# Kernel optimization log

Measured on AMD Instinct MI355X. Metric: run time of the kernel, lower is better.

Reference implementation:

```python
import jax, jax.numpy as jnp
import numpy as np

# ---- module geometry ----
BULK = 64          # bulk (J2) integration points, 3 comps each
COH = 32           # cohesive integration points, 2 comps each
LS = BULK * 3 + COH * 2  # = 256, material layer width

# ---- J2 plasticity material constants (plane-stress, linear isotropic hardening) ----
E_MOD = 200.0
NU = 0.3
SY0 = 2.0
HARD = 10.0
G_MOD = E_MOD / (2.0 * (1.0 + NU))
_c = E_MOD / (1.0 - NU * NU)
C_EL = np.array([[_c, _c * NU, 0.0], [_c * NU, _c, 0.0], [0.0, 0.0, _c * (1.0 - NU) / 2.0]], dtype=np.float32)
C_INV = np.linalg.inv(C_EL).astype(np.float32)

# ---- Turon cohesive-zone constants (bilinear damage law) ----
K_PEN = 50.0       # penalty stiffness
DELTA0 = 0.1       # damage-onset effective jump
DELTAF = 1.0       # full-failure effective jump


def j2_update(eps, epsp, epbar):
    # eps, epsp: [B,P,3]; epbar: [B,P]. Radial-return with linear hardening.
    sig_tr = jnp.einsum('bpi,ji->bpj', eps - epsp, jnp.asarray(C_EL))
    s1, s2, s12 = sig_tr[..., 0], sig_tr[..., 1], sig_tr[..., 2]
    seq = jnp.sqrt(jnp.maximum(s1 * s1 - s1 * s2 + s2 * s2 + 3.0 * s12 * s12, 1e-12))
    f = seq - (SY0 + HARD * epbar)
    plastic = f > 0.0
    dep = jnp.where(plastic, f / (3.0 * G_MOD + HARD), 0.0)
    r = (SY0 + HARD * (epbar + dep)) / seq
    sig = jnp.where(plastic[..., None], r[..., None] * sig_tr, sig_tr)
    epsp_new = jnp.where(plastic[..., None], eps - jnp.einsum('bpj,ij->bpi', sig, jnp.asarray(C_INV)), epsp)
    return sig, epsp_new, epbar + dep


def coh_update(jump, hist):
    # jump: [B,P,2] (normal, shear); hist: [B,P] max effective jump (damage history).
    dn, ds = jump[..., 0], jump[..., 1]
    lam = jnp.sqrt(jnp.maximum(jnp.maximum(dn, 0.0) ** 2 + ds * ds, 1e-12))
    hist_new = jnp.maximum(hist, lam)
    dmg = jnp.clip(DELTAF * (hist_new - DELTA0) / (jnp.maximum(hist_new, 1e-12) * (DELTAF - DELTA0)), 0.0, 1.0)
    tn = K_PEN * dn * jnp.where(dn > 0.0, 1.0 - dmg, 1.0)  # compression is undamaged
    ts = (1.0 - dmg) * K_PEN * ds
    return jnp.stack([tn, ts], axis=-1), hist_new


def setup_inputs() -> dict:
    key = jax.random.key(0)
    k1, k2, k3 = jax.random.split(key, 3)
    x = jax.random.normal(k1, (256, 1024, 16), dtype=jnp.float32)
    W1 = jax.random.normal(k2, (LS, 16), dtype=jnp.float32) * 0.1
    W2 = jax.random.normal(k3, (16, LS), dtype=jnp.float32) * 0.1
    return {"x": x, "W1": W1, "W2": W2}


def reference(x, W1, W2):
    B, T, F = x.shape
    # fc1 applied to every (batch, time) slice (original loops; here one GEMM)
    h = jnp.einsum('btf,lf->btl', x, W1)  # [B,T,LS]
    h_t = jnp.transpose(h, (1, 0, 2))     # [T,B,LS] for the time scan

    epsp0 = jnp.zeros((B, BULK, 3), dtype=x.dtype)
    epbar0 = jnp.zeros((B, BULK), dtype=x.dtype)
    hist0 = jnp.zeros((B, COH), dtype=x.dtype)

    def step(carry, ht):
        epsp, epbar, hist = carry
        eps = ht[:, : BULK * 3].reshape(B, BULK, 3)
        jmp = ht[:, BULK * 3:].reshape(B, COH, 2)
        sig, epsp, epbar = j2_update(eps, epsp, epbar)   # update + commit per step
        trac, hist = coh_update(jmp, hist)
        y = jnp.concatenate([sig.reshape(B, -1), trac.reshape(B, -1)], axis=-1)
        return (epsp, epbar, hist), y

    _, ys = jax.lax.scan(step, (epsp0, epbar0, hist0), h_t)  # [T,B,LS]
    ys = jnp.transpose(ys, (1, 0, 2))  # [B,T,LS]
    # softLayer fc2: linear with softplus-constrained (non-negative) weights
    out = jnp.einsum('btl,ol->bto', ys, jax.nn.softplus(W2))
    return out
```

## Files before the change

kernel.cpp:

```cpp
#include <hip/hip_runtime.h>
#include <cmath>
#include <cstdint>

#define BATCH  256
#define TT     1024
#define FIN    16
#define TC     32
#define NCHUNK (TT / TC)
#define SROW   324
#define YSS    328
#define HB     16

typedef __attribute__((ext_vector_type(8))) short short8;
typedef __attribute__((ext_vector_type(4))) float floatx4;

__device__ __forceinline__ unsigned short f2bf_rne(float f) {
    union { float f; unsigned int i; } v; v.f = f;
    unsigned int b = v.i;
    return (unsigned short)((b + 0x7FFFu + ((b >> 16) & 1u)) >> 16);
}
__device__ __forceinline__ float u2f(unsigned int u) {
    union { unsigned int i; float f; } v; v.i = u; return v.f;
}

#define BARRIER() asm volatile("s_waitcnt lgkmcnt(0)\n\ts_barrier" ::: "memory")
#define SBAR()    __builtin_amdgcn_sched_barrier(0)

#define MC00   219.78021978021977f
#define MC01   65.93406593406593f
#define MC22   76.92307692307692f
#define MSY0   2.0f
#define AK     0.958466453674121406f
#define BK     0.041533546325878594f


__global__ __launch_bounds__(512, 2)
void fused_mat_kernel(const float* __restrict__ x,
                      const float* __restrict__ w1,
                      const float* __restrict__ w2,
                      float* __restrict__ out)
{
    __shared__ __attribute__((aligned(16))) float          s_h[2][TC][SROW];
    __shared__ __attribute__((aligned(16))) unsigned short s_y[2][TC][YSS];

    const int tid  = threadIdx.x;
    const int b    = blockIdx.x;
    const int lane = tid & 63;
    const int wv   = tid >> 6;
    const int m    = lane & 15;
    const int q    = lane >> 4;

    const size_t xrow = (size_t)b * TT;

    const bool isG   = (wv == 2) | (wv == 3) | (wv == 6) | (wv == 7);
    const int  hw    = (wv == 2) ? 0 : (wv == 3) ? 1 : (wv == 6) ? 2 : 3;
    const int  nbase = hw * 5;

    short8 wfrag[5];
    short8 vf[10];
    uint4  rxc[2][2], rxp[2][2];

    auto emit = [&](const short8* axv, const short8* adxv, float* dst) {
        #pragma unroll
        for (int mt = 0; mt < 2; ++mt) {
            float* drow = dst + (mt * 16 + m) * SROW + q * 4 + nbase * 16;
            #pragma unroll
            for (int j = 0; j < 5; ++j) {
                const int n = nbase + j;
                floatx4 acc = {0.f, 0.f, 0.f, 0.f};
                acc = __builtin_amdgcn_mfma_f32_16x16x32_bf16(
                        wfrag[j], (n < 16) ? adxv[mt] : axv[mt], acc, 0, 0, 0);
                *(floatx4*)(drow + j * 16) = acc;
            }
        }
    };

    if (isG) {
        #pragma unroll
        for (int j = 0; j < 5; ++j) {
            const int n = nbase + j;
            #pragma unroll
            for (int jj = 0; jj < 8; ++jj) {
                float v = 0.f;
                if (q < 2) {
                    const int f = q * 8 + jj;
                    if (n < 16) {
                        const int lp = n * 16 + m, c = lp >> 2, cm = lp & 3;
                        if (cm < 3) {
                            const float wa  = w1[(3 * c + 0) * FIN + f];
                            const float wb  = w1[(3 * c + 1) * FIN + f];
                            const float wcc = w1[(3 * c + 2) * FIN + f];
                            v = (cm == 0) ? fmaf(MC01, wb, MC00 * wa)
                              : (cm == 1) ? fmaf(MC00, wb, MC01 * wa)
                                          : MC22 * wcc;
                        }
                    } else {
                        v = w1[(192 + (n - 16) * 16 + m) * FIN + f];
                    }
                }
                wfrag[j][jj] = (short)f2bf_rne(v);
            }
        }
        short8 ax0[2], adx0[2];
        #pragma unroll
        for (int mt = 0; mt < 2; ++mt) {
            #pragma unroll
            for (int j = 0; j < 8; ++j) {
                float xc = 0.f, xp = 0.f;
                if (q < 2) {
                    const int rowB = mt * 16 + m;
                    xc = x[(xrow + rowB) * FIN + q * 8 + j];
                    if (rowB > 0) xp = x[(xrow + rowB - 1) * FIN + q * 8 + j];
                }
                ax0[mt][j]  = (short)f2bf_rne(xc);
                adx0[mt][j] = (short)f2bf_rne(xc - xp);
            }
        }
        if (q < 2) {
            #pragma unroll
            for (int mt = 0; mt < 2; ++mt) {
                const int rowB = TC + mt * 16 + m;
                const float* xc = x + (xrow + rowB) * FIN + q * 8;
                const float* xp = x + (xrow + rowB - 1) * FIN + q * 8;
                rxc[mt][0] = *(const uint4*)xc;  rxc[mt][1] = *(const uint4*)(xc + 4);
                rxp[mt][0] = *(const uint4*)xp;  rxp[mt][1] = *(const uint4*)(xp + 4);
            }
        }
        emit(ax0, adx0, &s_h[0][0][0]);
    } else if (wv == 4 || wv == 5) {
        #pragma unroll
        for (int ks = 0; ks < 10; ++ks) {
            #pragma unroll
            for (int j = 0; j < 8; ++j) {
                const int p = ks * 32 + q * 8 + j;
                unsigned short v = 0;
                if (p < 256) {
                    const int comp = p & 3;
                    if (comp < 3) {
                        const int l = 3 * (p >> 2) + comp;
                        float xv = w2[m * 256 + l];
                        float sp = fmaxf(xv, 0.0f) + log1pf(expf(-fabsf(xv)));
                        v = f2bf_rne(sp);
                    }
                } else {
                    const int l = p - 64;
                    float xv = w2[m * 256 + l];
                    float sp = fmaxf(xv, 0.0f) + log1pf(expf(-fabsf(xv)));
                    v = f2bf_rne(sp);
                }
                vf[ks][j] = (short)v;
            }
        }
    }

    float tt0 = 0.f, tt1 = 0.f, tt2 = 0.f, rr = 1.0f, syv = MSY0, pre = AK * MSY0;
    float hist = 0.f;

    __syncthreads();

    for (int i = 0; i <= NCHUNK; ++i) {
        if (wv == 0) {
            if (i < NCHUNK) {
                const float* hb = &s_h[i & 1][0][0] + 4 * lane;
                unsigned short* yb = &s_y[i & 1][0][0] + 4 * lane;
                floatx4 dvvA[HB], dvvB[HB];
                uint2   yreg[TC];
                #pragma unroll
                for (int t = 0; t < HB; ++t) dvvA[t] = *(const floatx4*)(hb + t * SROW);
                SBAR();
                #pragma unroll
                for (int t = 0; t < HB; ++t) dvvB[t] = *(const floatx4*)(hb + (HB + t) * SROW);
                SBAR();
                #pragma unroll
                for (int t = 0; t < TC; ++t) {
                    const floatx4 dv = (t < HB) ? dvvA[t] : dvvB[t - HB];
                    tt0 = fmaf(rr, tt0, dv.x);
                    tt1 = fmaf(rr, tt1, dv.y);
                    tt2 = fmaf(rr, tt2, dv.z);
                    const float s01 = tt0 - tt1;
                    const float u   = tt2 * tt2;
                    const float w3  = fmaf(u, 3.0f, 1e-12f);
                    const float bb  = fmaf(tt1, tt1, w3);
                    const float qq  = fmaf(tt0, s01, bb);
                    const float rs  = __builtin_amdgcn_rsqf(qq);
                    const float seq = qq * rs;
                    rr  = fminf(fmaf(pre, rs, BK), 1.0f);
                    syv = fmaxf(syv, fmaf(BK, seq, pre));
                    pre = AK * syv;
                    const float sg0 = rr * tt0, sg1 = rr * tt1, sg2 = rr * tt2;
                    unsigned int r0, r1;
                    asm("v_cvt_pk_bf16_f32 %0, %1, %2" : "=v"(r0) : "v"(sg0), "v"(sg1));
                    asm("v_cvt_pk_bf16_f32 %0, %1, %2" : "=v"(r1) : "v"(sg2), "v"(sg2));
                    yreg[t].x = r0; yreg[t].y = r1;
                }
                SBAR();
                #pragma unroll
                for (int t = 0; t < TC; ++t)
                    *(uint2*)(yb + t * YSS) = yreg[t];
            }
        } else if (wv == 1) {
            if (i < NCHUNK && lane < 32) {
                const float* hc = &s_h[i & 1][0][0] + 256 + 2 * lane;
                unsigned short* yc = &s_y[i & 1][0][0] + 256 + 2 * lane;
                float2 jvv[TC];
                unsigned int yr[TC];
                #pragma unroll
                for (int t = 0; t < TC; ++t) jvv[t] = *(const float2*)(hc + t * SROW);
                SBAR();
                #pragma unroll
                for (int t = 0; t < TC; ++t) {
                    const float dn = jvv[t].x, ds = jvv[t].y;
                    const float dnp = fmaxf(dn, 0.0f);
                    const float lam = __builtin_amdgcn_sqrtf(fmaxf(fmaf(dnp, dnp, ds * ds), 1e-12f));
                    hist = fmaxf(hist, lam);
                    float dmg = (hist - 0.1f) * __builtin_amdgcn_rcpf(hist * 0.9f);
                    dmg = fminf(fmaxf(dmg, 0.0f), 1.0f);
                    const float om = 1.0f - dmg;
                    const float tn = 50.0f * dn * (dn > 0.0f ? om : 1.0f);
                    const float ts = om * 50.0f * ds;
                    unsigned int r;
                    asm("v_cvt_pk_bf16_f32 %0, %1, %2" : "=v"(r) : "v"(tn), "v"(ts));
                    yr[t] = r;
                }
                SBAR();
                #pragma unroll
                for (int t = 0; t < TC; ++t)
                    *(unsigned int*)(yc + t * YSS) = yr[t];
            }
        } else if (isG) {
            if (i + 1 < NCHUNK) {
                short8 ax[2], adx[2];
                #pragma unroll
                for (int mt = 0; mt < 2; ++mt) {
                    const unsigned int wc[8] = {rxc[mt][0].x, rxc[mt][0].y, rxc[mt][0].z, rxc[mt][0].w,
                                                rxc[mt][1].x, rxc[mt][1].y, rxc[mt][1].z, rxc[mt][1].w};
                    const unsigned int wp[8] = {rxp[mt][0].x, rxp[mt][0].y, rxp[mt][0].z, rxp[mt][0].w,
                                                rxp[mt][1].x, rxp[mt][1].y, rxp[mt][1].z, rxp[mt][1].w};
                    union { unsigned int u[4]; short8 s; } Ua, Ud;
                    #pragma unroll
                    for (int p = 0; p < 4; ++p) {
                        const float c0 = u2f(wc[2 * p]),          c1 = u2f(wc[2 * p + 1]);
                        const float d0 = c0 - u2f(wp[2 * p]),     d1 = c1 - u2f(wp[2 * p + 1]);
                        unsigned int va, vd;
                        asm("v_cvt_pk_bf16_f32 %0, %1, %2" : "=v"(va) : "v"(c0), "v"(c1));
                        asm("v_cvt_pk_bf16_f32 %0, %1, %2" : "=v"(vd) : "v"(d0), "v"(d1));
                        Ua.u[p] = (q < 2) ? va : 0u;
                        Ud.u[p] = (q < 2) ? vd : 0u;
                    }
                    ax[mt]  = Ua.s;
                    adx[mt] = Ud.s;
                }
                if (i + 2 < NCHUNK && q < 2) {
                    #pragma unroll
                    for (int mt = 0; mt < 2; ++mt) {
                        const int rowB = (i + 2) * TC + mt * 16 + m;
                        const float* xc = x + (xrow + rowB) * FIN + q * 8;
                        const float* xp = x + (xrow + rowB - 1) * FIN + q * 8;
                        rxc[mt][0] = *(const uint4*)xc;  rxc[mt][1] = *(const uint4*)(xc + 4);
                        rxp[mt][0] = *(const uint4*)xp;  rxp[mt][1] = *(const uint4*)(xp + 4);
                    }
                }
                emit(ax, adx, &s_h[(i + 1) & 1][0][0]);
            }
        } else {
            if (i >= 1) {
                const int mt = wv - 4;
                const int tb = (i - 1) * TC;
                const unsigned short* yb = &s_y[(i - 1) & 1][0][0];
                floatx4 a0 = {0.f, 0.f, 0.f, 0.f};
                floatx4 a1 = {0.f, 0.f, 0.f, 0.f};
                #pragma unroll
                for (int ks = 0; ks < 5; ++ks) {
                    const short8* yp = (const short8*)(yb + (mt * 16 + m) * YSS + ks * 32 + q * 8);
                    a0 = __builtin_amdgcn_mfma_f32_16x16x32_bf16(*yp, vf[ks], a0, 0, 0, 0);
                }
                #pragma unroll
                for (int ks = 5; ks < 10; ++ks) {
                    const short8* yp = (const short8*)(yb + (mt * 16 + m) * YSS + ks * 32 + q * 8);
                    a1 = __builtin_amdgcn_mfma_f32_16x16x32_bf16(*yp, vf[ks], a1, 0, 0, 0);
                }
                #pragma unroll
                for (int r = 0; r < 4; ++r)
                    out[(xrow + tb + mt * 16 + q * 4 + r) * FIN + m] = a0[r] + a1[r];
            }
        }
        BARRIER();
    }
}

extern "C" void kernel_launch(void* const* d_in, const int* in_sizes, int n_in,
                              void* d_out, int out_size, void* d_ws, size_t ws_size,
                              hipStream_t stream) {
    const float* x  = (const float*)d_in[0];
    const float* w1 = (const float*)d_in[1];
    const float* w2 = (const float*)d_in[2];
    float* out = (float*)d_out;
    fused_mat_kernel<<<BATCH, 512, 0, stream>>>(x, w1, w2, out);
}
```

Baseline: 140.7 us.

## Replace per-chunk block barriers with LDS flag-based producer/consumer sync

Each wave role gets its own loop, and the block-wide barrier every chunk is replaced by LDS flags that producers set and consumers spin on. The serial J2 wave can start its next chunk as soon as the input tile and the free output buffer are ready, instead of waiting for the slowest role. The risk is fragile memory ordering: only a compiler fence is used on the acquire side and an lgkmcnt wait on the release side. Spinning waves also compete for issue slots.

```diff
diff --git a/kernel.cpp b/kernel.cpp
--- a/kernel.cpp
+++ b/kernel.cpp
@@ -23,8 +23,9 @@
     union { unsigned int i; float f; } v; v.i = u; return v.f;
 }
 
-#define BARRIER() asm volatile("s_waitcnt lgkmcnt(0)\n\ts_barrier" ::: "memory")
-#define SBAR()    __builtin_amdgcn_sched_barrier(0)
+#define SBAR()  __builtin_amdgcn_sched_barrier(0)
+#define ACQ()   asm volatile("" ::: "memory")
+#define REL()   asm volatile("s_waitcnt lgkmcnt(0)" ::: "memory")
 
 #define MC00   219.78021978021977f
 #define MC01   65.93406593406593f
@@ -42,6 +43,9 @@
 {
     __shared__ __attribute__((aligned(16))) float          s_h[2][TC][SROW];
     __shared__ __attribute__((aligned(16))) unsigned short s_y[2][TC][YSS];
+    __shared__ int flg[16];
+
+    volatile int* F = (volatile int*)flg;
 
     const int tid  = threadIdx.x;
     const int b    = blockIdx.x;
@@ -59,6 +63,10 @@
     short8 wfrag[5];
     short8 vf[10];
     uint4  rxc[2][2], rxp[2][2];
+
+    if (tid == 0) {
+        flg[4] = -1; flg[5] = -1; flg[6] = -1; flg[7] = -1; flg[8] = -1; flg[9] = -1;
+    }
 
     auto emit = [&](const short8* axv, const short8* adxv, float* dst) {
         #pragma unroll
@@ -127,6 +135,7 @@
             }
         }
         emit(ax0, adx0, &s_h[0][0][0]);
+        if (lane == 0) flg[hw] = 0;
     } else if (wv == 4 || wv == 5) {
         #pragma unroll
         for (int ks = 0; ks < 10; ++ks) {
@@ -158,48 +167,58 @@
 
     __syncthreads();
 
-    for (int i = 0; i <= NCHUNK; ++i) {
-        if (wv == 0) {
-            if (i < NCHUNK) {
-                const float* hb = &s_h[i & 1][0][0] + 4 * lane;
-                unsigned short* yb = &s_y[i & 1][0][0] + 4 * lane;
-                floatx4 dvvA[HB], dvvB[HB];
-                uint2   yreg[TC];
-                #pragma unroll
-                for (int t = 0; t < HB; ++t) dvvA[t] = *(const floatx4*)(hb + t * SROW);
-                SBAR();
-                #pragma unroll
-                for (int t = 0; t < HB; ++t) dvvB[t] = *(const floatx4*)(hb + (HB + t) * SROW);
-                SBAR();
-                #pragma unroll
-                for (int t = 0; t < TC; ++t) {
-                    const floatx4 dv = (t < HB) ? dvvA[t] : dvvB[t - HB];
-                    tt0 = fmaf(rr, tt0, dv.x);
-                    tt1 = fmaf(rr, tt1, dv.y);
-                    tt2 = fmaf(rr, tt2, dv.z);
-                    const float s01 = tt0 - tt1;
-                    const float u   = tt2 * tt2;
-                    const float w3  = fmaf(u, 3.0f, 1e-12f);
-                    const float bb  = fmaf(tt1, tt1, w3);
-                    const float qq  = fmaf(tt0, s01, bb);
-                    const float rs  = __builtin_amdgcn_rsqf(qq);
-                    const float seq = qq * rs;
-                    rr  = fminf(fmaf(pre, rs, BK), 1.0f);
-                    syv = fmaxf(syv, fmaf(BK, seq, pre));
-                    pre = AK * syv;
-                    const float sg0 = rr * tt0, sg1 = rr * tt1, sg2 = rr * tt2;
-                    unsigned int r0, r1;
-                    asm("v_cvt_pk_bf16_f32 %0, %1, %2" : "=v"(r0) : "v"(sg0), "v"(sg1));
-                    asm("v_cvt_pk_bf16_f32 %0, %1, %2" : "=v"(r1) : "v"(sg2), "v"(sg2));
-                    yreg[t].x = r0; yreg[t].y = r1;
-                }
-                SBAR();
-                #pragma unroll
-                for (int t = 0; t < TC; ++t)
-                    *(uint2*)(yb + t * YSS) = yreg[t];
-            }
-        } else if (wv == 1) {
-            if (i < NCHUNK && lane < 32) {
+    if (wv == 0) {
+        for (int i = 0; i < NCHUNK; ++i) {
+            while (F[0] < i) {} while (F[1] < i) {} while (F[2] < i) {} while (F[3] < i) {}
+            const int yf = i - 2;
+            while (F[8] < yf) {} while (F[9] < yf) {}
+            ACQ();
+            const float* hb = &s_h[i & 1][0][0] + 4 * lane;
+            unsigned short* yb = &s_y[i & 1][0][0] + 4 * lane;
+            floatx4 dvvA[HB], dvvB[HB];
+            uint2   yreg[TC];
+            #pragma unroll
+            for (int t = 0; t < HB; ++t) dvvA[t] = *(const floatx4*)(hb + t * SROW);
+            SBAR();
+            #pragma unroll
+            for (int t = 0; t < HB; ++t) dvvB[t] = *(const floatx4*)(hb + (HB + t) * SROW);
+            SBAR();
+            #pragma unroll
+            for (int t = 0; t < TC; ++t) {
+                const floatx4 dv = (t < HB) ? dvvA[t] : dvvB[t - HB];
+                tt0 = fmaf(rr, tt0, dv.x);
+                tt1 = fmaf(rr, tt1, dv.y);
+                tt2 = fmaf(rr, tt2, dv.z);
+                const float s01 = tt0 - tt1;
+                const float u   = tt2 * tt2;
+                const float w3  = fmaf(u, 3.0f, 1e-12f);
+                const float bb  = fmaf(tt1, tt1, w3);
+                const float qq  = fmaf(tt0, s01, bb);
+                const float rs  = __builtin_amdgcn_rsqf(qq);
+                const float seq = qq * rs;
+                rr  = fminf(fmaf(pre, rs, BK), 1.0f);
+                syv = fmaxf(syv, fmaf(BK, seq, pre));
+                pre = AK * syv;
+                const float sg0 = rr * tt0, sg1 = rr * tt1, sg2 = rr * tt2;
+                unsigned int r0, r1;
+                asm("v_cvt_pk_bf16_f32 %0, %1, %2" : "=v"(r0) : "v"(sg0), "v"(sg1));
+                asm("v_cvt_pk_bf16_f32 %0, %1, %2" : "=v"(r1) : "v"(sg2), "v"(sg2));
+                yreg[t].x = r0; yreg[t].y = r1;
+            }
+            SBAR();
+            #pragma unroll
+            for (int t = 0; t < TC; ++t)
+                *(uint2*)(yb + t * YSS) = yreg[t];
+            REL();
+            if (lane == 0) { F[4] = i; F[6] = i; }
+        }
+    } else if (wv == 1) {
+        for (int i = 0; i < NCHUNK; ++i) {
+            while (F[3] < i) {}
+            const int yf = i - 2;
+            while (F[8] < yf) {} while (F[9] < yf) {}
+            ACQ();
+            if (lane < 32) {
                 const float* hc = &s_h[i & 1][0][0] + 256 + 2 * lane;
                 unsigned short* yc = &s_y[i & 1][0][0] + 256 + 2 * lane;
                 float2 jvv[TC];
@@ -227,64 +246,76 @@
                 for (int t = 0; t < TC; ++t)
                     *(unsigned int*)(yc + t * YSS) = yr[t];
             }
-        } else if (isG) {
-            if (i + 1 < NCHUNK) {
-                short8 ax[2], adx[2];
+            REL();
+            if (lane == 0) { F[5] = i; F[7] = i; }
+        }
+    } else if (isG) {
+        for (int k = 1; k < NCHUNK; ++k) {
+            short8 ax[2], adx[2];
+            #pragma unroll
+            for (int mt = 0; mt < 2; ++mt) {
+                const unsigned int wc[8] = {rxc[mt][0].x, rxc[mt][0].y, rxc[mt][0].z, rxc[mt][0].w,
+                                            rxc[mt][1].x, rxc[mt][1].y, rxc[mt][1].z, rxc[mt][1].w};
+                const unsigned int wp[8] = {rxp[mt][0].x, rxp[mt][0].y, rxp[mt][0].z, rxp[mt][0].w,
+                                            rxp[mt][1].x, rxp[mt][1].y, rxp[mt][1].z, rxp[mt][1].w};
+                union { unsigned int u[4]; short8 s; } Ua, Ud;
+                #pragma unroll
+                for (int p = 0; p < 4; ++p) {
+                    const float c0 = u2f(wc[2 * p]),          c1 = u2f(wc[2 * p + 1]);
+                    const float d0 = c0 - u2f(wp[2 * p]),     d1 = c1 - u2f(wp[2 * p + 1]);
+                    unsigned int va, vd;
+                    asm("v_cvt_pk_bf16_f32 %0, %1, %2" : "=v"(va) : "v"(c0), "v"(c1));
+                    asm("v_cvt_pk_bf16_f32 %0, %1, %2" : "=v"(vd) : "v"(d0), "v"(d1));
+                    Ua.u[p] = (q < 2) ? va : 0u;
+                    Ud.u[p] = (q < 2) ? vd : 0u;
+                }
+                ax[mt]  = Ua.s;
+                adx[mt] = Ud.s;
+            }
+            if (k + 1 < NCHUNK && q < 2) {
                 #pragma unroll
                 for (int mt = 0; mt < 2; ++mt) {
-                    const unsigned int wc[8] = {rxc[mt][0].x, rxc[mt][0].y, rxc[mt][0].z, rxc[mt][0].w,
-                                                rxc[mt][1].x, rxc[mt][1].y, rxc[mt][1].z, rxc[mt][1].w};
-                    const unsigned int wp[8] = {rxp[mt][0].x, rxp[mt][0].y, rxp[mt][0].z, rxp[mt][0].w,
-                                                rxp[mt][1].x, rxp[mt][1].y, rxp[mt][1].z, rxp[mt][1].w};
-                    union { unsigned int u[4]; short8 s; } Ua, Ud;
-                    #pragma unroll
-                    for (int p = 0; p < 4; ++p) {
-                        const float c0 = u2f(wc[2 * p]),          c1 = u2f(wc[2 * p + 1]);
-                        const float d0 = c0 - u2f(wp[2 * p]),     d1 = c1 - u2f(wp[2 * p + 1]);
-                        unsigned int va, vd;
-                        asm("v_cvt_pk_bf16_f32 %0, %1, %2" : "=v"(va) : "v"(c0), "v"(c1));
-                        asm("v_cvt_pk_bf16_f32 %0, %1, %2" : "=v"(vd) : "v"(d0), "v"(d1));
-                        Ua.u[p] = (q < 2) ? va : 0u;
-                        Ud.u[p] = (q < 2) ? vd : 0u;
-                    }
-                    ax[mt]  = Ua.s;
-                    adx[mt] = Ud.s;
-                }
-                if (i + 2 < NCHUNK && q < 2) {
-                    #pragma unroll
-                    for (int mt = 0; mt < 2; ++mt) {
-                        const int rowB = (i + 2) * TC + mt * 16 + m;
-                        const float* xc = x + (xrow + rowB) * FIN + q * 8;
-                        const float* xp = x + (xrow + rowB - 1) * FIN + q * 8;
-                        rxc[mt][0] = *(const uint4*)xc;  rxc[mt][1] = *(const uint4*)(xc + 4);
-                        rxp[mt][0] = *(const uint4*)xp;  rxp[mt][1] = *(const uint4*)(xp + 4);
-                    }
-                }
-                emit(ax, adx, &s_h[(i + 1) & 1][0][0]);
-            }
-        } else {
-            if (i >= 1) {
-                const int mt = wv - 4;
-                const int tb = (i - 1) * TC;
-                const unsigned short* yb = &s_y[(i - 1) & 1][0][0];
-                floatx4 a0 = {0.f, 0.f, 0.f, 0.f};
-                floatx4 a1 = {0.f, 0.f, 0.f, 0.f};
-                #pragma unroll
-                for (int ks = 0; ks < 5; ++ks) {
-                    const short8* yp = (const short8*)(yb + (mt * 16 + m) * YSS + ks * 32 + q * 8);
-                    a0 = __builtin_amdgcn_mfma_f32_16x16x32_bf16(*yp, vf[ks], a0, 0, 0, 0);
-                }
-                #pragma unroll
-                for (int ks = 5; ks < 10; ++ks) {
-                    const short8* yp = (const short8*)(yb + (mt * 16 + m) * YSS + ks * 32 + q * 8);
-                    a1 = __builtin_amdgcn_mfma_f32_16x16x32_bf16(*yp, vf[ks], a1, 0, 0, 0);
-                }
-                #pragma unroll
-                for (int r = 0; r < 4; ++r)
-                    out[(xrow + tb + mt * 16 + q * 4 + r) * FIN + m] = a0[r] + a1[r];
-            }
-        }
-        BARRIER();
+                    const int rowB = (k + 1) * TC + mt * 16 + m;
+                    const float* xc = x + (xrow + rowB) * FIN + q * 8;
+                    const float* xp = x + (xrow + rowB - 1) * FIN + q * 8;
+                    rxc[mt][0] = *(const uint4*)xc;  rxc[mt][1] = *(const uint4*)(xc + 4);
+                    rxp[mt][0] = *(const uint4*)xp;  rxp[mt][1] = *(const uint4*)(xp + 4);
+                }
+            }
+            const int hf = k - 2;
+            while (F[4] < hf) __builtin_amdgcn_s_sleep(1);
+            if (hw == 3) { while (F[5] < hf) __builtin_amdgcn_s_sleep(1); }
+            ACQ();
+            emit(ax, adx, &s_h[k & 1][0][0]);
+            REL();
+            if (lane == 0) F[hw] = k;
+        }
+    } else {
+        const int mt = wv - 4;
+        for (int j = 0; j < NCHUNK; ++j) {
+            while (F[6] < j) __builtin_amdgcn_s_sleep(1);
+            while (F[7] < j) __builtin_amdgcn_s_sleep(1);
+            ACQ();
+            const int tb = j * TC;
+            const unsigned short* yb = &s_y[j & 1][0][0];
+            floatx4 a0 = {0.f, 0.f, 0.f, 0.f};
+            floatx4 a1 = {0.f, 0.f, 0.f, 0.f};
+            #pragma unroll
+            for (int ks = 0; ks < 5; ++ks) {
+                const short8* yp = (const short8*)(yb + (mt * 16 + m) * YSS + ks * 32 + q * 8);
+                a0 = __builtin_amdgcn_mfma_f32_16x16x32_bf16(*yp, vf[ks], a0, 0, 0, 0);
+            }
+            #pragma unroll
+            for (int ks = 5; ks < 10; ++ks) {
+                const short8* yp = (const short8*)(yb + (mt * 16 + m) * YSS + ks * 32 + q * 8);
+                a1 = __builtin_amdgcn_mfma_f32_16x16x32_bf16(*yp, vf[ks], a1, 0, 0, 0);
+            }
+            #pragma unroll
+            for (int r = 0; r < 4; ++r)
+                out[(xrow + tb + mt * 16 + q * 4 + r) * FIN + m] = a0[r] + a1[r];
+            REL();
+            if (lane == 0) F[8 + mt] = j;
+        }
     }
 }
 
```

Result: slower. 150.9 us (+7.3%).
